# Kernel tuning notes

Measured on AMD Instinct MI355X. Metric: run time of the kernel, lower is better.

Reference implementation:

```python
import jax, jax.numpy as jnp
import numpy as np


def setup_inputs() -> dict:
    key = jax.random.key(0)
    ks = jax.random.split(key, 8)
    B, C, H, W = 4, 512, 64, 64
    C8 = C // 8
    return {
        "x": jax.random.normal(ks[0], (B, C, H, W), dtype=jnp.float32),
        "Wq": jax.random.normal(ks[1], (C8, C), dtype=jnp.float32) * 0.02,
        "bq": jax.random.normal(ks[2], (C8,), dtype=jnp.float32) * 0.02,
        "Wk": jax.random.normal(ks[3], (C8, C), dtype=jnp.float32) * 0.02,
        "bk": jax.random.normal(ks[4], (C8,), dtype=jnp.float32) * 0.02,
        "Wv": jax.random.normal(ks[5], (C, C), dtype=jnp.float32) * 0.02,
        "bv": jax.random.normal(ks[6], (C,), dtype=jnp.float32) * 0.02,
        "gamma": jax.random.normal(ks[7], (1,), dtype=jnp.float32),
    }


def reference(x, Wq, bq, Wk, bk, Wv, bv, gamma):
    B, C, H, W = x.shape
    N = H * W
    xf = x.reshape(B, C, N)  # 1x1 conv == per-position matmul over channels
    q = jnp.einsum('oc,bcn->bno', Wq, xf) + bq  # B, N, C//8  (proj_query^T)
    k = jnp.einsum('oc,bcn->bon', Wk, xf) + bk[None, :, None]  # B, C//8, N
    v = jnp.einsum('oc,bcn->bon', Wv, xf) + bv[None, :, None]  # B, C, N
    energy = jnp.einsum('bno,bom->bnm', q, k)  # B, N, N
    attention = jax.nn.softmax(energy, axis=-1)
    # out = bmm(proj_value, attention^T): out[:, :, n] = sum_m v[:, :, m] * att[n, m]
    out = jnp.einsum('bcm,bnm->bcn', v, attention).reshape(B, C, H, W)
    return gamma[0] * out + x
```

## Files before the change

### kernel.cpp

```cpp
#include <hip/hip_runtime.h>
#include <stdint.h>


typedef unsigned short u16;
typedef unsigned char u8;
typedef __attribute__((ext_vector_type(8))) short short8;
typedef __attribute__((ext_vector_type(4))) float f32x4;
typedef __attribute__((ext_vector_type(16))) float f32x16;
typedef __attribute__((ext_vector_type(4))) int i32x4;
typedef __attribute__((ext_vector_type(8))) int i32x8;

#define ASYNC16(gp, lp)                                                        \
  __builtin_amdgcn_global_load_lds(                                            \
      (__attribute__((address_space(1))) void*)(void*)(gp),                    \
      (__attribute__((address_space(3))) void*)(lp), 16, 0, 0)

#define WAIT_VM0 0x0F70
#define WAIT_VM3 0x0F73
#define WAIT_VM4 0x0F74
#define WAIT_LGKM0 0xC07F

#define EXP_SHIFT 5.0f
#define EXP_CAP 57000.0f

__device__ __forceinline__ u16 f2bf(float f) {
  uint32_t u = __float_as_uint(f);
  u += 0x7FFFu + ((u >> 16) & 1u);
  return (u16)(u >> 16);
}

__device__ __forceinline__ u8 f2fp8(float f) {
  f = fminf(fmaxf(f, -440.f), 440.f);
  int r = __builtin_amdgcn_cvt_pk_fp8_f32(f, f, 0, false);
  return (u8)(r & 0xFF);
}

__global__ __launch_bounds__(256) void k_transpose(const float* __restrict__ x,
                                                   u16* __restrict__ xT) {
  __shared__ float tile[64][65];
  const int b = blockIdx.z;
  const int nb = blockIdx.x * 64;
  const int cb = blockIdx.y * 64;
  const int t = threadIdx.x;
  {
    const int nl = (t & 15) * 4, c0 = t >> 4;
    const float* xp = x + ((size_t)b * 512 + cb) * 4096 + nb;
#pragma unroll
    for (int p = 0; p < 4; ++p) {
      const int cl = c0 + p * 16;
      const float4 v = *(const float4*)(xp + (size_t)cl * 4096 + nl);
      tile[cl][nl] = v.x;
      tile[cl][nl + 1] = v.y;
      tile[cl][nl + 2] = v.z;
      tile[cl][nl + 3] = v.w;
    }
  }
  __syncthreads();
  {
    const int cl = (t & 15) * 4, n0 = t >> 4;
    u16* xtp = xT + ((size_t)b * 4096 + nb) * 512 + cb;
#pragma unroll
    for (int p = 0; p < 4; ++p) {
      const int nl = n0 + p * 16;
      ushort4 o;
      o.x = f2bf(tile[cl][nl]);
      o.y = f2bf(tile[cl + 1][nl]);
      o.z = f2bf(tile[cl + 2][nl]);
      o.w = f2bf(tile[cl + 3][nl]);
      *(ushort4*)(xtp + (size_t)nl * 512 + cl) = o;
    }
  }
}

__global__ __launch_bounds__(256) void k_wcast(const float* __restrict__ Wq,
                                               const float* __restrict__ Wk,
                                               const float* __restrict__ Wv,
                                               u16* __restrict__ wqk,
                                               u16* __restrict__ wv) {
  const int idx = blockIdx.x * 256 + threadIdx.x;
  if (idx < 128 * 512) {
    const int r = idx >> 9, c = idx & 511;
    const float f = (r < 64) ? Wq[r * 512 + c] : Wk[(r - 64) * 512 + c];
    wqk[idx] = f2bf(f);
  } else {
    const int j = idx - 128 * 512;
    if (j < 512 * 512) wv[j] = f2bf(Wv[j]);
  }
}

__device__ __forceinline__ void gemm8_bt(const u16* __restrict__ A,
                                         const u16* __restrict__ B,
                                         const int K, const int rowA0,
                                         const int colB0, u16* smem,
                                         f32x4 acc[4][2]) {
  const int t = threadIdx.x;
  const int lane = t & 63, w = t >> 6;
  const int quad = lane >> 4, l15 = lane & 15;
  const int wr = w >> 2, wc = w & 3;
  const f32x4 zero = {0.f, 0.f, 0.f, 0.f};
#pragma unroll
  for (int i = 0; i < 4; ++i)
#pragma unroll
    for (int j = 0; j < 2; ++j) acc[i][j] = zero;

  const int srow = t >> 3;
  const int c8 = (lane & 7) ^ (lane >> 3);
  const u16* ga = A + (size_t)(rowA0 + srow) * K + c8 * 8;
  const u16* gb = B + (size_t)(colB0 + srow) * K + c8 * 8;
  const size_t rK64 = (size_t)64 * K;

#define STAGE_G(bi, k0)                                                        \
  do {                                                                         \
    char* Ab = (char*)smem + (bi) * 32768 + w * 1024;                          \
    char* Bb = (char*)smem + (bi) * 32768 + 16384 + w * 1024;                  \
    ASYNC16(ga + (k0), Ab);                                                    \
    ASYNC16(ga + (k0) + rK64, Ab + 8192);                                      \
    ASYNC16(gb + (k0), Bb);                                                    \
    ASYNC16(gb + (k0) + rK64, Bb + 8192);                                      \
  } while (0)

  const int sw0 = (quad) ^ (l15 & 7);
  const int sw1 = (4 + quad) ^ (l15 & 7);

  const int nIt = K >> 6;
  STAGE_G(0, 0);
  STAGE_G(1, 64);

  for (int it = 0; it < nIt; ++it) {
    if (it < nIt - 1)
      __builtin_amdgcn_s_waitcnt(WAIT_VM4);
    else
      __builtin_amdgcn_s_waitcnt(WAIT_VM0);
    asm volatile("" ::: "memory");
    __builtin_amdgcn_s_barrier();
    asm volatile("" ::: "memory");

    const u16* As = smem + (it & 1) * 16384;
    const u16* Bs = As + 8192;
#pragma unroll
    for (int s = 0; s < 2; ++s) {
      const int sw = s ? sw1 : sw0;
      short8 a[4], b[2];
#pragma unroll
      for (int i = 0; i < 4; ++i)
        a[i] = *(const short8*)(As + (wr * 64 + i * 16 + l15) * 64 + sw * 8);
#pragma unroll
      for (int j = 0; j < 2; ++j)
        b[j] = *(const short8*)(Bs + (wc * 32 + j * 16 + l15) * 64 + sw * 8);
      __builtin_amdgcn_s_setprio(1);
#pragma unroll
      for (int i = 0; i < 4; ++i)
#pragma unroll
        for (int j = 0; j < 2; ++j)
          acc[i][j] = __builtin_amdgcn_mfma_f32_16x16x32_bf16(a[i], b[j],
                                                              acc[i][j], 0, 0, 0);
      __builtin_amdgcn_s_setprio(0);
    }
    asm volatile("" ::: "memory");
    __builtin_amdgcn_s_barrier();
    asm volatile("" ::: "memory");
    if (it + 2 < nIt) STAGE_G(it & 1, (it + 2) * 64);
  }
#undef STAGE_G
}

__global__ __launch_bounds__(512, 4) void k_proj(const u16* __restrict__ xT,
                                                 const u16* __restrict__ wqk,
                                                 const u16* __restrict__ wv,
                                                 const float* __restrict__ bq,
                                                 const float* __restrict__ bk,
                                                 const float* __restrict__ bv,
                                                 u16* __restrict__ q,
                                                 u16* __restrict__ kT,
                                                 u8* __restrict__ v8) {
  __shared__ u16 smem[32768];
  const int b = blockIdx.z;
  const int by = blockIdx.y;
  const int t = threadIdx.x, lane = t & 63, w = t >> 6;
  const int quad = lane >> 4, l15 = lane & 15;
  const int wr = w >> 2, wc = w & 3;
  f32x4 acc[4][2];

  if (by == 4) {
    const int rowA0 = blockIdx.x * 128;
    gemm8_bt(xT + (size_t)b * 4096 * 512, wqk, 512, rowA0, 0, smem, acc);
#pragma unroll
    for (int j = 0; j < 2; ++j) {
      const int col = wc * 32 + j * 16 + l15;
      const float bias = (col < 64) ? bq[col] : bk[col - 64];
#pragma unroll
      for (int i = 0; i < 4; ++i) {
#pragma unroll
        for (int r = 0; r < 4; ++r) {
          const int row = rowA0 + wr * 64 + i * 16 + quad * 4 + r;
          const float val = acc[i][j][r] + bias;
          if (col < 64)
            q[((size_t)b * 4096 + row) * 64 + col] = f2bf(val);
          else
            kT[((size_t)b * 4096 + row) * 64 + (col - 64)] = f2bf(val);
        }
      }
    }
  } else {
    const int rowA0 = by * 128;
    const int colB0 = blockIdx.x * 128;
    gemm8_bt(wv, xT + (size_t)b * 4096 * 512, 512, rowA0, colB0, smem, acc);
#pragma unroll
    for (int i = 0; i < 4; ++i) {
#pragma unroll
      for (int r = 0; r < 4; ++r) {
        const int row = rowA0 + wr * 64 + i * 16 + quad * 4 + r;
        const float bias = bv[row];
#pragma unroll
        for (int j = 0; j < 2; ++j) {
          const int col = colB0 + wc * 32 + j * 16 + l15;
          v8[((size_t)b * 512 + row) * 4096 + col] = f2fp8(acc[i][j][r] + bias);
        }
      }
    }
  }
}

__global__ __launch_bounds__(1024, 4) void k_fused(
    const u16* __restrict__ q, const u16* __restrict__ kT,
    const u8* __restrict__ v8, const float* __restrict__ x,
    const float* __restrict__ gamma, float* __restrict__ out) {
  __shared__ u16 k_lds[2][128 * 64];
  __shared__ u8 v_lds[2][2][256 * 64];
  __shared__ u8 P_lds[2][128 * 64];
  __shared__ float lsum_lds[8][128];

  const int t = threadIdx.x;
  const int l = t & 63, w = t >> 6;
  const int quad = l >> 4, l15 = l & 15;
  const int l31 = l & 31, h = l >> 5;

  const int n0 = blockIdx.x * 128;
  const int c0 = blockIdx.y * 256;
  const int b = blockIdx.z;

  const u16* qg = q + ((size_t)b * 4096 + n0) * 64;
  const u16* kg = kT + (size_t)b * 4096 * 64;
  const u8* vg = v8 + ((size_t)b * 512 + c0) * 4096;

  const int kr = t >> 3, kc = t & 7;
  const u16* qsg = qg + kr * 64 + (kc ^ (kr & 7)) * 8;
  const u16* ksg = kg + kr * 64 + (kc ^ (kr & 7)) * 8;
  const int vr = t >> 2, va = t & 3;
  const u8* vsg = vg + (size_t)vr * 4096 + (va ^ ((vr >> 1) & 3)) * 16;

#define STAGE_F(bi, m0)                                                        \
  do {                                                                         \
    ASYNC16(ksg + (size_t)(m0) * 64, (char*)k_lds[bi] + w * 1024);             \
    ASYNC16(vsg + (m0), (char*)v_lds[bi][0] + w * 1024);                       \
    ASYNC16(vsg + (m0) + 64, (char*)v_lds[bi][1] + w * 1024);                  \
  } while (0)

  ASYNC16(qsg, (char*)P_lds[0] + w * 1024);
  STAGE_F(0, 0);
  __builtin_amdgcn_s_waitcnt(WAIT_VM3);
  __builtin_amdgcn_s_barrier();
  asm volatile("" ::: "memory");
  const int ms = w >> 1, nh = w & 1;
  const int sw0 = quad ^ (l15 & 7);
  const int sw1 = (4 + quad) ^ (l15 & 7);
  short8 af[4][2];
#pragma unroll
  for (int s = 0; s < 4; ++s) {
    const u16* qrow = (const u16*)P_lds[0] + (nh * 64 + s * 16 + l15) * 64;
    af[s][0] = *(const short8*)(qrow + sw0 * 8);
    af[s][1] = *(const short8*)(qrow + sw1 * 8);
  }
  asm volatile("" ::: "memory");
  __builtin_amdgcn_s_waitcnt(WAIT_LGKM0);
  __builtin_amdgcn_s_barrier();
  asm volatile("" ::: "memory");

  const int wrp = w >> 2, wcp = w & 3;
  int rowA[2], sA1[2], sA2[2];
#pragma unroll
  for (int i = 0; i < 2; ++i) {
    rowA[i] = wrp * 64 + i * 32 + l31;
    const int fa = (rowA[i] >> 1) & 3;
    sA1[i] = (2 * h) ^ fa;
    sA2[i] = (2 * h + 1) ^ fa;
  }
  const int rowB = wcp * 32 + l31;
  const int fbB = (rowB >> 1) & 3;
  const int sB1 = (2 * h) ^ fbB;
  const int sB2 = (2 * h + 1) ^ fbB;

  const int fbW = (l15 >> 1) & 3;
  u8* Pwbase = P_lds[ms >> 2] + (nh * 64 + l15) * 64 +
               (((ms & 3) ^ fbW) * 16) + quad * 4;

  const int krow_off = (ms * 16 + l15) * 64;

  f32x16 acc[2];
#pragma unroll
  for (int i = 0; i < 2; ++i)
#pragma unroll
    for (int r = 0; r < 16; ++r) acc[i][r] = 0.f;

  float lsums[4] = {0.f, 0.f, 0.f, 0.f};
  const f32x4 zero = {0.f, 0.f, 0.f, 0.f};

  for (int it = 0; it < 32; ++it) {
    __builtin_amdgcn_s_waitcnt(WAIT_VM0);
    asm volatile("" ::: "memory");
    __builtin_amdgcn_s_barrier();
    asm volatile("" ::: "memory");
    const int cur = it & 1;
    if (it + 1 < 32) STAGE_F(cur ^ 1, (it + 1) * 128);

    const u16* kb = k_lds[cur];
    const short8 kf0 = *(const short8*)(kb + krow_off + sw0 * 8);
    const short8 kf1 = *(const short8*)(kb + krow_off + sw1 * 8);
    f32x4 eacc[4];
#pragma unroll
    for (int s = 0; s < 4; ++s) eacc[s] = zero;
    __builtin_amdgcn_s_setprio(1);
#pragma unroll
    for (int s = 0; s < 4; ++s)
      eacc[s] = __builtin_amdgcn_mfma_f32_16x16x32_bf16(kf0, af[s][0],
                                                        eacc[s], 0, 0, 0);
#pragma unroll
    for (int s = 0; s < 4; ++s)
      eacc[s] = __builtin_amdgcn_mfma_f32_16x16x32_bf16(kf1, af[s][1],
                                                        eacc[s], 0, 0, 0);
    __builtin_amdgcn_s_setprio(0);

#pragma unroll
    for (int s = 0; s < 4; ++s) {
      const float e0 = fminf(__expf(eacc[s][0] - EXP_SHIFT), EXP_CAP);
      const float e1 = fminf(__expf(eacc[s][1] - EXP_SHIFT), EXP_CAP);
      const float e2 = fminf(__expf(eacc[s][2] - EXP_SHIFT), EXP_CAP);
      const float e3 = fminf(__expf(eacc[s][3] - EXP_SHIFT), EXP_CAP);
      lsums[s] += (e0 + e1) + (e2 + e3);
      int pk = __builtin_amdgcn_cvt_pk_bf8_f32(e0, e1, 0, false);
      pk = __builtin_amdgcn_cvt_pk_bf8_f32(e2, e3, pk, true);
      *(int*)(Pwbase + s * 1024) = pk;
    }
    asm volatile("" ::: "memory");
    __builtin_amdgcn_s_waitcnt(WAIT_LGKM0);
    __builtin_amdgcn_s_barrier();
    asm volatile("" ::: "memory");

#pragma unroll
    for (int ks = 0; ks < 2; ++ks) {
      const u8* Vb = v_lds[cur][ks];
      const u8* Pb = P_lds[ks];
      i32x8 bb;
      {
        const u8* pb = Pb + rowB * 64;
        const i32x4 blo = *(const i32x4*)(pb + sB1 * 16);
        const i32x4 bhi = *(const i32x4*)(pb + sB2 * 16);
        bb[0] = blo[0]; bb[1] = blo[1]; bb[2] = blo[2]; bb[3] = blo[3];
        bb[4] = bhi[0]; bb[5] = bhi[1]; bb[6] = bhi[2]; bb[7] = bhi[3];
      }
      __builtin_amdgcn_s_setprio(1);
#pragma unroll
      for (int i = 0; i < 2; ++i) {
        const u8* pa = Vb + rowA[i] * 64;
        const i32x4 lo = *(const i32x4*)(pa + sA1[i] * 16);
        const i32x4 hi = *(const i32x4*)(pa + sA2[i] * 16);
        i32x8 a;
        a[0] = lo[0]; a[1] = lo[1]; a[2] = lo[2]; a[3] = lo[3];
        a[4] = hi[0]; a[5] = hi[1]; a[6] = hi[2]; a[7] = hi[3];
        acc[i] = __builtin_amdgcn_mfma_scale_f32_32x32x64_f8f6f4(
            a, bb, acc[i], 0 , 1 , 0, 0x7F, 0, 0x7F);
      }
      __builtin_amdgcn_s_setprio(0);
    }
    asm volatile("" ::: "memory");
  }
#undef STAGE_F

#pragma unroll
  for (int s = 0; s < 4; ++s) {
    lsums[s] += __shfl_xor(lsums[s], 16);
    lsums[s] += __shfl_xor(lsums[s], 32);
  }
  if (l < 16) {
#pragma unroll
    for (int s = 0; s < 4; ++s)
      lsum_lds[ms][nh * 64 + s * 16 + l] = lsums[s];
  }
  asm volatile("" ::: "memory");
  __builtin_amdgcn_s_waitcnt(WAIT_LGKM0);
  __builtin_amdgcn_s_barrier();
  asm volatile("" ::: "memory");

  const float g = gamma[0];
  const int col = n0 + wcp * 32 + l31;
  const int nc = wcp * 32 + l31;
  float den = 0.f;
#pragma unroll
  for (int m = 0; m < 8; ++m) den += lsum_lds[m][nc];
  const float gil = g / den;
#pragma unroll
  for (int i = 0; i < 2; ++i) {
#pragma unroll
    for (int r = 0; r < 16; ++r) {
      const int rloc = (r & 3) + 8 * (r >> 2) + 4 * h;
      const int row = c0 + wrp * 64 + i * 32 + rloc;
      const size_t idx = ((size_t)b * 512 + row) * 4096 + col;
      out[idx] = gil * acc[i][r] + x[idx];
    }
  }
}

extern "C" void kernel_launch(void* const* d_in, const int* in_sizes, int n_in,
                              void* d_out, int out_size, void* d_ws,
                              size_t ws_size, hipStream_t stream) {
  const float* x = (const float*)d_in[0];
  const float* Wq = (const float*)d_in[1];
  const float* bq = (const float*)d_in[2];
  const float* Wk = (const float*)d_in[3];
  const float* bk = (const float*)d_in[4];
  const float* Wv = (const float*)d_in[5];
  const float* bv = (const float*)d_in[6];
  const float* gamma = (const float*)d_in[7];
  float* out = (float*)d_out;

  char* ws = (char*)d_ws;
  u16* xT = (u16*)(ws);
  u16* wqk = (u16*)(ws + 16777216);
  u16* wv = (u16*)(ws + 16908288);
  u16* qb = (u16*)(ws + 17432576);
  u16* ktb = (u16*)(ws + 19529728);
  u8* v8 = (u8*)(ws + 21626880);

  k_transpose<<<dim3(64, 8, 4), 256, 0, stream>>>(x, xT);
  k_wcast<<<dim3(1280), 256, 0, stream>>>(Wq, Wk, Wv, wqk, wv);
  k_proj<<<dim3(32, 5, 4), 512, 0, stream>>>(xT, wqk, wv, bq, bk, bv,
                                             qb, ktb, v8);
  k_fused<<<dim3(32, 2, 4), 1024, 0, stream>>>(qb, ktb, v8, x, gamma, out);
}
```

Measured before the change: 189.8 us.

## Software-pipeline QK energy and PV matmul stages with double-buffered P tile

```diff
diff --git a/kernel.cpp b/kernel.cpp
--- a/kernel.cpp
+++ b/kernel.cpp
@@ -16,7 +16,6 @@
       (__attribute__((address_space(3))) void*)(lp), 16, 0, 0)
 
 #define WAIT_VM0 0x0F70
-#define WAIT_VM3 0x0F73
 #define WAIT_VM4 0x0F74
 #define WAIT_LGKM0 0xC07F
 
@@ -128,7 +127,7 @@
 
   for (int it = 0; it < nIt; ++it) {
     if (it < nIt - 1)
-      __builtin_amdgcn_s_waitcnt(WAIT_VM4);
+      __builtin_amdgcn_s_waitcnt(0x0F74);
     else
       __builtin_amdgcn_s_waitcnt(WAIT_VM0);
     asm volatile("" ::: "memory");
@@ -227,7 +226,7 @@
     const float* __restrict__ gamma, float* __restrict__ out) {
   __shared__ u16 k_lds[2][128 * 64];
   __shared__ u8 v_lds[2][2][256 * 64];
-  __shared__ u8 P_lds[2][128 * 64];
+  __shared__ u8 P_lds[2][2][8192];
   __shared__ float lsum_lds[8][128];
 
   const int t = threadIdx.x;
@@ -249,16 +248,19 @@
   const int vr = t >> 2, va = t & 3;
   const u8* vsg = vg + (size_t)vr * 4096 + (va ^ ((vr >> 1) & 3)) * 16;
 
-#define STAGE_F(bi, m0)                                                        \
+#define STAGE_K(bi, m0)                                                        \
+  ASYNC16(ksg + (size_t)(m0) * 64, (char*)k_lds[bi] + w * 1024)
+#define STAGE_V(bi, m0)                                                        \
   do {                                                                         \
-    ASYNC16(ksg + (size_t)(m0) * 64, (char*)k_lds[bi] + w * 1024);             \
     ASYNC16(vsg + (m0), (char*)v_lds[bi][0] + w * 1024);                       \
     ASYNC16(vsg + (m0) + 64, (char*)v_lds[bi][1] + w * 1024);                  \
   } while (0)
 
-  ASYNC16(qsg, (char*)P_lds[0] + w * 1024);
-  STAGE_F(0, 0);
-  __builtin_amdgcn_s_waitcnt(WAIT_VM3);
+  ASYNC16(qsg, (char*)&P_lds[0][0][0] + w * 1024);
+  STAGE_K(0, 0);
+  STAGE_V(0, 0);
+  STAGE_K(1, 128);
+  __builtin_amdgcn_s_waitcnt(WAIT_VM4);
   __builtin_amdgcn_s_barrier();
   asm volatile("" ::: "memory");
   const int ms = w >> 1, nh = w & 1;
@@ -267,12 +269,13 @@
   short8 af[4][2];
 #pragma unroll
   for (int s = 0; s < 4; ++s) {
-    const u16* qrow = (const u16*)P_lds[0] + (nh * 64 + s * 16 + l15) * 64;
+    const u16* qrow = (const u16*)&P_lds[0][0][0] + (nh * 64 + s * 16 + l15) * 64;
     af[s][0] = *(const short8*)(qrow + sw0 * 8);
     af[s][1] = *(const short8*)(qrow + sw1 * 8);
   }
   asm volatile("" ::: "memory");
   __builtin_amdgcn_s_waitcnt(WAIT_LGKM0);
+  __builtin_amdgcn_s_waitcnt(WAIT_VM0);
   __builtin_amdgcn_s_barrier();
   asm volatile("" ::: "memory");
 
@@ -291,7 +294,7 @@
   const int sB2 = (2 * h + 1) ^ fbB;
 
   const int fbW = (l15 >> 1) & 3;
-  u8* Pwbase = P_lds[ms >> 2] + (nh * 64 + l15) * 64 +
+  u8* Pwbase = &P_lds[0][ms >> 2][0] + (nh * 64 + l15) * 64 +
                (((ms & 3) ^ fbW) * 16) + quad * 4;
 
   const int krow_off = (ms * 16 + l15) * 64;
@@ -305,76 +308,81 @@
   float lsums[4] = {0.f, 0.f, 0.f, 0.f};
   const f32x4 zero = {0.f, 0.f, 0.f, 0.f};
 
-  for (int it = 0; it < 32; ++it) {
-    __builtin_amdgcn_s_waitcnt(WAIT_VM0);
-    asm volatile("" ::: "memory");
-    __builtin_amdgcn_s_barrier();
-    asm volatile("" ::: "memory");
-    const int cur = it & 1;
-    if (it + 1 < 32) STAGE_F(cur ^ 1, (it + 1) * 128);
-
-    const u16* kb = k_lds[cur];
-    const short8 kf0 = *(const short8*)(kb + krow_off + sw0 * 8);
-    const short8 kf1 = *(const short8*)(kb + krow_off + sw1 * 8);
-    f32x4 eacc[4];
-#pragma unroll
-    for (int s = 0; s < 4; ++s) eacc[s] = zero;
-    __builtin_amdgcn_s_setprio(1);
-#pragma unroll
-    for (int s = 0; s < 4; ++s)
-      eacc[s] = __builtin_amdgcn_mfma_f32_16x16x32_bf16(kf0, af[s][0],
-                                                        eacc[s], 0, 0, 0);
-#pragma unroll
-    for (int s = 0; s < 4; ++s)
-      eacc[s] = __builtin_amdgcn_mfma_f32_16x16x32_bf16(kf1, af[s][1],
-                                                        eacc[s], 0, 0, 0);
-    __builtin_amdgcn_s_setprio(0);
-
-#pragma unroll
-    for (int s = 0; s < 4; ++s) {
-      const float e0 = fminf(__expf(eacc[s][0] - EXP_SHIFT), EXP_CAP);
-      const float e1 = fminf(__expf(eacc[s][1] - EXP_SHIFT), EXP_CAP);
-      const float e2 = fminf(__expf(eacc[s][2] - EXP_SHIFT), EXP_CAP);
-      const float e3 = fminf(__expf(eacc[s][3] - EXP_SHIFT), EXP_CAP);
-      lsums[s] += (e0 + e1) + (e2 + e3);
-      int pk = __builtin_amdgcn_cvt_pk_bf8_f32(e0, e1, 0, false);
-      pk = __builtin_amdgcn_cvt_pk_bf8_f32(e2, e3, pk, true);
-      *(int*)(Pwbase + s * 1024) = pk;
-    }
-    asm volatile("" ::: "memory");
-    __builtin_amdgcn_s_waitcnt(WAIT_LGKM0);
-    __builtin_amdgcn_s_barrier();
-    asm volatile("" ::: "memory");
-
-#pragma unroll
-    for (int ks = 0; ks < 2; ++ks) {
-      const u8* Vb = v_lds[cur][ks];
-      const u8* Pb = P_lds[ks];
-      i32x8 bb;
-      {
-        const u8* pb = Pb + rowB * 64;
-        const i32x4 blo = *(const i32x4*)(pb + sB1 * 16);
-        const i32x4 bhi = *(const i32x4*)(pb + sB2 * 16);
-        bb[0] = blo[0]; bb[1] = blo[1]; bb[2] = blo[2]; bb[3] = blo[3];
-        bb[4] = bhi[0]; bb[5] = bhi[1]; bb[6] = bhi[2]; bb[7] = bhi[3];
+  for (int j = 0; j <= 32; ++j) {
+    if (j > 0) {
+      __builtin_amdgcn_s_waitcnt(WAIT_LGKM0);
+      __builtin_amdgcn_s_waitcnt(WAIT_VM0);
+      asm volatile("" ::: "memory");
+      __builtin_amdgcn_s_barrier();
+      asm volatile("" ::: "memory");
+      if (j < 32) STAGE_V(j & 1, j * 128);
+      if (j + 1 < 32) STAGE_K((j + 1) & 1, (j + 1) * 128);
+    }
+
+    if (j < 32) {
+      const u16* kb = k_lds[j & 1];
+      const short8 kf0 = *(const short8*)(kb + krow_off + sw0 * 8);
+      const short8 kf1 = *(const short8*)(kb + krow_off + sw1 * 8);
+      f32x4 eacc[4];
+#pragma unroll
+      for (int s = 0; s < 4; ++s) eacc[s] = zero;
+      __builtin_amdgcn_s_setprio(1);
+#pragma unroll
+      for (int s = 0; s < 4; ++s)
+        eacc[s] = __builtin_amdgcn_mfma_f32_16x16x32_bf16(kf0, af[s][0],
+                                                          eacc[s], 0, 0, 0);
+#pragma unroll
+      for (int s = 0; s < 4; ++s)
+        eacc[s] = __builtin_amdgcn_mfma_f32_16x16x32_bf16(kf1, af[s][1],
+                                                          eacc[s], 0, 0, 0);
+      __builtin_amdgcn_s_setprio(0);
+
+      u8* Pw = Pwbase + (j & 1) * 16384;
+#pragma unroll
+      for (int s = 0; s < 4; ++s) {
+        const float e0 = fminf(__expf(eacc[s][0] - EXP_SHIFT), EXP_CAP);
+        const float e1 = fminf(__expf(eacc[s][1] - EXP_SHIFT), EXP_CAP);
+        const float e2 = fminf(__expf(eacc[s][2] - EXP_SHIFT), EXP_CAP);
+        const float e3 = fminf(__expf(eacc[s][3] - EXP_SHIFT), EXP_CAP);
+        lsums[s] += (e0 + e1) + (e2 + e3);
+        int pk = __builtin_amdgcn_cvt_pk_bf8_f32(e0, e1, 0, false);
+        pk = __builtin_amdgcn_cvt_pk_bf8_f32(e2, e3, pk, true);
+        *(int*)(Pw + s * 1024) = pk;
       }
-      __builtin_amdgcn_s_setprio(1);
-#pragma unroll
-      for (int i = 0; i < 2; ++i) {
-        const u8* pa = Vb + rowA[i] * 64;
-        const i32x4 lo = *(const i32x4*)(pa + sA1[i] * 16);
-        const i32x4 hi = *(const i32x4*)(pa + sA2[i] * 16);
-        i32x8 a;
-        a[0] = lo[0]; a[1] = lo[1]; a[2] = lo[2]; a[3] = lo[3];
-        a[4] = hi[0]; a[5] = hi[1]; a[6] = hi[2]; a[7] = hi[3];
-        acc[i] = __builtin_amdgcn_mfma_scale_f32_32x32x64_f8f6f4(
-            a, bb, acc[i], 0 , 1 , 0, 0x7F, 0, 0x7F);
+    }
+
+    if (j > 0) {
+      const int pc = (j - 1) & 1;
+#pragma unroll
+      for (int ks = 0; ks < 2; ++ks) {
+        const u8* Vb = v_lds[pc][ks];
+        const u8* Pb = &P_lds[pc][ks][0];
+        i32x8 bb;
+        {
+          const u8* pb = Pb + rowB * 64;
+          const i32x4 blo = *(const i32x4*)(pb + sB1 * 16);
+          const i32x4 bhi = *(const i32x4*)(pb + sB2 * 16);
+          bb[0] = blo[0]; bb[1] = blo[1]; bb[2] = blo[2]; bb[3] = blo[3];
+          bb[4] = bhi[0]; bb[5] = bhi[1]; bb[6] = bhi[2]; bb[7] = bhi[3];
+        }
+        __builtin_amdgcn_s_setprio(1);
+#pragma unroll
+        for (int i = 0; i < 2; ++i) {
+          const u8* pa = Vb + rowA[i] * 64;
+          const i32x4 lo = *(const i32x4*)(pa + sA1[i] * 16);
+          const i32x4 hi = *(const i32x4*)(pa + sA2[i] * 16);
+          i32x8 a;
+          a[0] = lo[0]; a[1] = lo[1]; a[2] = lo[2]; a[3] = lo[3];
+          a[4] = hi[0]; a[5] = hi[1]; a[6] = hi[2]; a[7] = hi[3];
+          acc[i] = __builtin_amdgcn_mfma_scale_f32_32x32x64_f8f6f4(
+              a, bb, acc[i], 0 , 1 , 0, 0x7F, 0, 0x7F);
+        }
+        __builtin_amdgcn_s_setprio(0);
       }
-      __builtin_amdgcn_s_setprio(0);
-    }
-    asm volatile("" ::: "memory");
-  }
-#undef STAGE_F
+    }
+  }
+#undef STAGE_K
+#undef STAGE_V
 
 #pragma unroll
   for (int s = 0; s < 4; ++s) {
```

Result: faster. 180.2 us (-5.1%).
